# Performance work log

Hardware: AMD Instinct MI355X
Metric: run time of the kernel (lower is better)

Reference implementation:

```python
import jax, jax.numpy as jnp
import numpy as np

N_NODES = 100000
N_EDGES = 1600000
HID = 150
N_LAYERS = 5


def setup_inputs() -> dict:
    key = jax.random.key(0)
    ks = jax.random.split(key, 7)
    s = 1.0 / np.sqrt(HID)
    return {
        "x": jax.random.normal(ks[0], (N_NODES, HID), dtype=jnp.float32),
        "weight": jax.random.uniform(ks[1], (N_LAYERS, HID, HID), jnp.float32, -s, s),
        "w_ih": jax.random.uniform(ks[2], (3 * HID, HID), jnp.float32, -s, s),
        "w_hh": jax.random.uniform(ks[3], (3 * HID, HID), jnp.float32, -s, s),
        "b_ih": jax.random.uniform(ks[4], (3 * HID,), jnp.float32, -s, s),
        "b_hh": jax.random.uniform(ks[5], (3 * HID,), jnp.float32, -s, s),
        "edge_index": jax.random.randint(ks[6], (2, N_EDGES), 0, N_NODES, dtype=jnp.int32),
    }


def _gru_cell(inp, h, w_ih, w_hh, b_ih, b_hh):
    # torch.nn.GRUCell math
    gi = inp @ w_ih.T + b_ih            # [N, 3H]
    gh = h @ w_hh.T + b_hh              # [N, 3H]
    i_r, i_z, i_n = jnp.split(gi, 3, axis=-1)
    h_r, h_z, h_n = jnp.split(gh, 3, axis=-1)
    r = jax.nn.sigmoid(i_r + h_r)
    z = jax.nn.sigmoid(i_z + h_z)
    n = jnp.tanh(i_n + r * h_n)
    return (1.0 - z) * n + z * h


def reference(x, weight, w_ih, w_hh, b_ih, b_hh, edge_index):
    # GatedGraphConv: h'_i = GRU( sum_{j->i} (h_j @ W_l), h_i ), repeated num_layers times
    src, dst = edge_index[0], edge_index[1]
    n_nodes = x.shape[0]
    h = x
    for l in range(weight.shape[0]):
        m = h @ weight[l]                                        # [N, H] transform
        aggr = jax.ops.segment_sum(m[src], dst, num_segments=n_nodes)  # scatter-add over edges
        h = _gru_cell(aggr, h, w_ih, w_hh, b_ih, b_hh)
    return h
```

## Files before the change

kernel.cpp:

```cpp
#include <hip/hip_runtime.h>
#include <hip/hip_bf16.h>
#include <cmath>

#define HID 150
#define NN 100000
#define NE 1600000
#define NL 5
#define G3 (3*HID)
#define KP 320
#define NP 640
#define KS 10
#define BM 64
#define HSTEPS 20
#define HS_BF (20*64*8)

#define NPBSH 9
#define NBK 196
#define CAPL 64
#define CAPG 10240
#define CHUNK 4096
#define BPAD 16

typedef __hip_bfloat16 bf16;
using short8 = __attribute__((ext_vector_type(8))) short;
using f32x4  = __attribute__((ext_vector_type(4))) float;

static __device__ __forceinline__ unsigned short bf_bits(float v) {
    __hip_bfloat16 h = __float2bfloat16(v);
    return *reinterpret_cast<unsigned short*>(&h);
}

static __device__ __forceinline__ float blo(unsigned int p) {
    return __uint_as_float((p & 0xffffu) << 16);
}
static __device__ __forceinline__ float bhi(unsigned int p) {
    return __uint_as_float(p & 0xffff0000u);
}

static __device__ __forceinline__ void gld_lds16(const void* g, void* l) {
    __builtin_amdgcn_global_load_lds(
        (const __attribute__((address_space(1))) void*)g,
        (__attribute__((address_space(3))) void*)l, 16, 0, 0);
}

__global__ void build_wfrag(const float* __restrict__ W, const float* __restrict__ w_ih,
                            const float* __restrict__ w_hh, const float* __restrict__ b_ih,
                            const float* __restrict__ b_hh, bf16* __restrict__ wfrag) {
    int idx = blockIdx.x * 256 + threadIdx.x;
    if (idx >= NL * KP * NP) return;
    int j = idx % NP;
    int k = (idx / NP) % KP;
    int l = idx / (NP * KP);
    int sec = j / 160;
    int f = j - sec * 160;
    float v = 0.f;
    if (f < HID) {
        if (k < HID) {
            if (sec < 3) {
                const float* Wl = W + (size_t)l * HID * HID + (size_t)k * HID;
                const float* wr = w_ih + (size_t)(sec * HID + f) * HID;
                float acc = 0.f;
                for (int t = 0; t < HID; ++t) acc += Wl[t] * wr[t];
                v = acc;
            }
        } else if (k == HID) {
            v = (sec == 0) ? b_ih[f] + b_hh[f]
              : (sec == 1) ? b_ih[HID + f] + b_hh[HID + f]
              : (sec == 2) ? b_ih[2 * HID + f]
                           : b_hh[2 * HID + f];
        } else if (k >= 160 && k < 160 + HID) {
            int kk = k - 160;
            if (sec == 0)      v = w_hh[(size_t)f * HID + kk];
            else if (sec == 1) v = w_hh[(size_t)(HID + f) * HID + kk];
            else if (sec == 3) v = w_hh[(size_t)(2 * HID + f) * HID + kk];
        }
    }
    int kstep = k >> 5, kq = (k >> 3) & 3, ki = k & 7;
    int half = sec >> 1, s2 = sec & 1;
    int fgroup = f >> 4, nl = j & 15;
    int tl = s2 * 10 + fgroup;
    int lane = kq * 16 + nl;
    size_t addr = ((((size_t)(l * KS + kstep) * 2 + half) * 20 + tl) * 64 + lane) * 8 + ki;
    wfrag[addr] = __float2bfloat16(v);
}

__global__ __launch_bounds__(256)
void bin_edges(const int* __restrict__ ei, int* __restrict__ bcnt,
               unsigned int* __restrict__ bbuf) {
    __shared__ int lcnt[NBK];
    __shared__ unsigned int lstage[NBK * CAPL];
    int t = threadIdx.x;
    for (int i = t; i < NBK; i += 256) lcnt[i] = 0;
    __syncthreads();
    int e0 = blockIdx.x * CHUNK;
#pragma unroll
    for (int it = 0; it < CHUNK / 256; ++it) {
        int e = e0 + it * 256 + t;
        if (e < NE) {
            int src = ei[e], dst = ei[NE + e];
            int b = dst >> NPBSH;
            unsigned int v = (unsigned int)src | ((unsigned int)(dst & 511) << 17);
            int li = atomicAdd(&lcnt[b], 1);
            if (li < CAPL) {
                lstage[b * CAPL + li] = v;
            } else {
                int gp = atomicAdd(&bcnt[b * BPAD], 1);
                if (gp < CAPG) bbuf[(size_t)b * CAPG + gp] = v;
            }
        }
    }
    __syncthreads();
    int wave = t >> 6, lane = t & 63;
    for (int b = wave; b < NBK; b += 4) {
        int cnt = lcnt[b];
        if (cnt > CAPL) cnt = CAPL;
        if (cnt == 0) continue;
        int base = 0;
        if (lane == 0) base = atomicAdd(&bcnt[b * BPAD], cnt);
        base = __shfl(base, 0, 64);
        if (lane < cnt && base + lane < CAPG)
            bbuf[(size_t)b * CAPG + base + lane] = lstage[b * CAPL + lane];
    }
}

__global__ __launch_bounds__(256)
void csr_from_buckets(const int* __restrict__ bcnt, const unsigned int* __restrict__ bbuf,
                      int* __restrict__ off, int* __restrict__ csr) {
    __shared__ int hist[512];
    __shared__ int s[256];
    int b = blockIdx.x, t = threadIdx.x;
    hist[t] = 0;
    hist[256 + t] = 0;
    int base = 0;
    for (int i = 0; i < b; ++i) {
        int c = bcnt[i * BPAD];
        base += (c > CAPG) ? CAPG : c;
    }
    int cnt = bcnt[b * BPAD];
    if (cnt > CAPG) cnt = CAPG;
    __syncthreads();
    for (int i = t; i < cnt; i += 256) {
        unsigned int v = bbuf[(size_t)b * CAPG + i];
        atomicAdd(&hist[v >> 17], 1);
    }
    __syncthreads();
    int a0 = hist[2 * t], a1 = hist[2 * t + 1];
    int tsum = a0 + a1;
    s[t] = tsum;
    __syncthreads();
    for (int d = 1; d < 256; d <<= 1) {
        int u = (t >= d) ? s[t - d] : 0;
        __syncthreads();
        s[t] += u;
        __syncthreads();
    }
    int tb = base + s[t] - tsum;
    hist[2 * t] = tb;
    hist[2 * t + 1] = tb + a0;
    int node = (b << NPBSH) + 2 * t;
    if (node < NN) off[node] = tb;
    if (node + 1 < NN) off[node + 1] = tb + a0;
    if (b == NBK - 1 && t == 255) off[NN] = base + s[255];
    __syncthreads();
    for (int i = t; i < cnt; i += 256) {
        unsigned int v = bbuf[(size_t)b * CAPG + i];
        int p = atomicAdd(&hist[v >> 17], 1);
        csr[p] = (int)(v & 0x1FFFFu);
    }
}

__global__ void init_h(const float* __restrict__ x, bf16* __restrict__ Abuf) {
    size_t i = (size_t)blockIdx.x * 256 + threadIdx.x;
    if (i >= (size_t)NN * HID) return;
    int m = (int)(i / HID), f = (int)(i - (size_t)m * HID);
    Abuf[(size_t)m * KP + 160 + f] = __float2bfloat16(x[i]);
}

__global__ void aggregate(bf16* __restrict__ Abuf, const int* __restrict__ off,
                          const int* __restrict__ csr) {
    int node = (blockIdx.x * blockDim.x + threadIdx.x) >> 6;
    int lane = threadIdx.x & 63;
    if (node >= NN) return;
    int e0 = off[node], e1 = off[node + 1];
    float a0 = 0.f, a1 = 0.f, b0 = 0.f, b1 = 0.f;
    bool tail = lane < 11;
    int e = e0;
    for (; e + 4 <= e1; e += 4) {
        const unsigned int* r0 = (const unsigned int*)(Abuf + (size_t)csr[e]     * KP + 160);
        const unsigned int* r1 = (const unsigned int*)(Abuf + (size_t)csr[e + 1] * KP + 160);
        const unsigned int* r2 = (const unsigned int*)(Abuf + (size_t)csr[e + 2] * KP + 160);
        const unsigned int* r3 = (const unsigned int*)(Abuf + (size_t)csr[e + 3] * KP + 160);
        unsigned int p0 = r0[lane], p1 = r1[lane], p2 = r2[lane], p3 = r3[lane];
        unsigned int q0 = 0, q1 = 0, q2 = 0, q3 = 0;
        if (tail) { q0 = r0[64 + lane]; q1 = r1[64 + lane]; q2 = r2[64 + lane]; q3 = r3[64 + lane]; }
        a0 += blo(p0) + blo(p1) + blo(p2) + blo(p3);
        a1 += bhi(p0) + bhi(p1) + bhi(p2) + bhi(p3);
        b0 += blo(q0) + blo(q1) + blo(q2) + blo(q3);
        b1 += bhi(q0) + bhi(q1) + bhi(q2) + bhi(q3);
    }
    for (; e < e1; ++e) {
        const unsigned int* r = (const unsigned int*)(Abuf + (size_t)csr[e] * KP + 160);
        unsigned int p = r[lane];
        unsigned int q = tail ? r[64 + lane] : 0;
        a0 += blo(p); a1 += bhi(p);
        b0 += blo(q); b1 += bhi(q);
    }
    unsigned int* out = (unsigned int*)(Abuf + (size_t)node * KP);
    out[lane] = (unsigned int)bf_bits(a0) | ((unsigned int)bf_bits(a1) << 16);
    if (tail) out[64 + lane] = (unsigned int)bf_bits(b0) | ((unsigned int)bf_bits(b1) << 16);
    if (lane < 5) out[75 + lane] = (lane == 0) ? 0x00003F80u : 0u;
}

__global__ __launch_bounds__(256, 2)
void gemm_gru(const bf16* __restrict__ Abuf, const bf16* __restrict__ wfrag_l,
              float* __restrict__ h_out, bf16* __restrict__ Abuf_w, int last) {
    __shared__ __align__(16) bf16 Bs[3][HS_BF];
    __shared__ __align__(16) bf16 As3[3][BM * 32];
    int tid = threadIdx.x;
    int wave = tid >> 6, lane = tid & 63;
    int mh = wave >> 1, nh = wave & 1;
    int row0 = blockIdx.x * BM;

    const char* gbase = (const char*)(Abuf + (size_t)row0 * KP);
    int ar = tid >> 2, aq = tid & 3;

    auto stageB = [&](int hs) {
        const char* gb = (const char*)(wfrag_l + (size_t)hs * HS_BF);
        char* lb = (char*)Bs[hs % 3];
#pragma unroll
        for (int it = 0; it < 5; ++it) {
            int c = it * 256 + tid;
            gld_lds16(gb + (size_t)c * 16, lb + (size_t)c * 16);
        }
    };
    auto stageA = [&](int ks) {
        gld_lds16(gbase + (size_t)ar * (KP * 2) + ks * 64 + aq * 16,
                  (char*)As3[ks % 3] + (size_t)tid * 16);
    };

    stageB(0); stageA(0); stageB(1); stageA(1);

    f32x4 acc[2][20];
#pragma unroll
    for (int mt = 0; mt < 2; ++mt)
#pragma unroll
        for (int t = 0; t < 20; ++t) acc[mt][t] = (f32x4){0.f, 0.f, 0.f, 0.f};

    int col = lane & 15, q = lane >> 4;
    short8 a0, a1;
#pragma unroll
    for (int hs = 0; hs < HSTEPS; ++hs) {
        if (hs < 18)       asm volatile("s_waitcnt vmcnt(6)" ::: "memory");
        else if (hs == 18) asm volatile("s_waitcnt vmcnt(5)" ::: "memory");
        else               asm volatile("s_waitcnt vmcnt(0)" ::: "memory");
        __builtin_amdgcn_s_barrier();
        __builtin_amdgcn_sched_barrier(0);

        int ks = hs >> 1, half = hs & 1, cur = hs % 3;
        if (half == 0) {
            const bf16* Ak = As3[ks % 3];
            a0 = *(const short8*)(Ak + ((mh * 32 + col) * 32 + q * 8));
            a1 = *(const short8*)(Ak + ((mh * 32 + 16 + col) * 32 + q * 8));
        }
#pragma unroll
        for (int g = 0; g < 5; ++g) {
#pragma unroll
            for (int s2 = 0; s2 < 2; ++s2) {
                int tl = s2 * 10 + nh * 5 + g;
                short8 b = *(const short8*)(Bs[cur] + ((size_t)(tl * 64 + lane) * 8));
                int t = g * 4 + half * 2 + s2;
                acc[0][t] = __builtin_amdgcn_mfma_f32_16x16x32_bf16(a0, b, acc[0][t], 0, 0, 0);
                acc[1][t] = __builtin_amdgcn_mfma_f32_16x16x32_bf16(a1, b, acc[1][t], 0, 0, 0);
            }
        }
        if (hs + 2 < HSTEPS) stageB(hs + 2);
        if (half == 1 && ks + 2 < KS) stageA(ks + 2);
    }

    int qrow = q * 4;
    bf16* Cs = &Bs[0][0];
#pragma unroll
    for (int mt = 0; mt < 2; ++mt) {
#pragma unroll
        for (int g = 0; g < 5; ++g) {
            int f = (nh * 5 + g) * 16 + col;
            if (f < HID) {
                f32x4 ar4 = acc[mt][g * 4 + 0], az = acc[mt][g * 4 + 1];
                f32x4 an = acc[mt][g * 4 + 2], ah = acc[mt][g * 4 + 3];
#pragma unroll
                for (int v = 0; v < 4; ++v) {
                    int rl = mh * 32 + mt * 16 + qrow + v;
                    float hp = __bfloat162float(Abuf[(size_t)(row0 + rl) * KP + 160 + f]);
                    float r = 1.f / (1.f + __expf(-ar4[v]));
                    float z = 1.f / (1.f + __expf(-az[v]));
                    float n = tanhf(an[v] + r * ah[v]);
                    float ho = (1.f - z) * n + z * hp;
                    if (last) {
                        int m = row0 + rl;
                        if (m < NN) h_out[(size_t)m * HID + f] = ho;
                    } else {
                        Cs[rl * 160 + f] = __float2bfloat16(ho);
                    }
                }
            }
        }
    }
    if (!last) {
        __syncthreads();
        const unsigned int* src = (const unsigned int*)Cs;
        for (int i = tid; i < 64 * 75; i += 256) {
            int r = i / 75, dw = i - r * 75;
            ((unsigned int*)(Abuf_w + (size_t)(row0 + r) * KP + 160))[dw] =
                src[r * 80 + dw];
        }
    }
}

extern "C" void kernel_launch(void* const* d_in, const int* in_sizes, int n_in,
                              void* d_out, int out_size, void* d_ws, size_t ws_size,
                              hipStream_t stream) {
    const float* x      = (const float*)d_in[0];
    const float* weight = (const float*)d_in[1];
    const float* w_ih   = (const float*)d_in[2];
    const float* w_hh   = (const float*)d_in[3];
    const float* b_ih   = (const float*)d_in[4];
    const float* b_hh   = (const float*)d_in[5];
    const int*   ei     = (const int*)d_in[6];
    float* h = (float*)d_out;

    const int nblk = (NN + BM - 1) / BM;
    const size_t NNP = (size_t)nblk * BM;
    char* p = (char*)d_ws;
    auto alloc = [&](size_t bytes) { char* r = p; p += (bytes + 255) & ~255ull; return r; };
    int*  off   = (int*)alloc((size_t)(NN + 1) * 4);
    int*  csr   = (int*)alloc((size_t)NE * 4);
    int*  bcnt  = (int*)alloc((size_t)NBK * BPAD * 4);
    unsigned int* bbuf = (unsigned int*)alloc((size_t)NBK * CAPG * 4);
    bf16* wfrag = (bf16*)alloc((size_t)NL * KS * 2 * HS_BF * 2);
    bf16* Abuf  = (bf16*)alloc((NNP + BM) * (size_t)KP * 2);

    hipMemsetAsync(bcnt, 0, (size_t)NBK * BPAD * 4, stream);
    build_wfrag<<<(NL * KP * NP + 255) / 256, 256, 0, stream>>>(weight, w_ih, w_hh, b_ih, b_hh, wfrag);
    bin_edges<<<(NE + CHUNK - 1) / CHUNK, 256, 0, stream>>>(ei, bcnt, bbuf);
    csr_from_buckets<<<NBK, 256, 0, stream>>>(bcnt, bbuf, off, csr);
    init_h<<<(int)(((size_t)NN * HID + 255) / 256), 256, 0, stream>>>(x, Abuf);

    for (int l = 0; l < NL; ++l) {
        aggregate<<<(NN * 64 + 255) / 256, 256, 0, stream>>>(Abuf, off, csr);
        gemm_gru<<<nblk, 256, 0, stream>>>(Abuf, wfrag + (size_t)l * KS * 2 * HS_BF,
                                           h, Abuf, (l == NL - 1) ? 1 : 0);
    }
}
```

Baseline: 1.111 ms.

## Double GEMM-GRU tile to 128 rows with 512 threads and pairwise B staging

Raises the gemm_gru row tile from 64 to 128 and the block from 256 to 512 threads, so each staged weight slice feeds twice as many rows. Weight fragments are now staged two half-steps at a time, which halves the number of barriers and waitcnts in the main loop. tanhf is replaced by an exp-based formula. The larger LDS footprint and one block per CU reduce occupancy, and the wave-to-tile mapping (mh from wave>>1) must now cover 8 waves correctly.

```diff
diff --git a/kernel.cpp b/kernel.cpp
--- a/kernel.cpp
+++ b/kernel.cpp
@@ -10,7 +10,7 @@
 #define KP 320
 #define NP 640
 #define KS 10
-#define BM 64
+#define BM 128
 #define HSTEPS 20
 #define HS_BF (20*64*8)
 
@@ -211,10 +211,10 @@
     if (lane < 5) out[75 + lane] = (lane == 0) ? 0x00003F80u : 0u;
 }
 
-__global__ __launch_bounds__(256, 2)
+__global__ __launch_bounds__(512, 1)
 void gemm_gru(const bf16* __restrict__ Abuf, const bf16* __restrict__ wfrag_l,
               float* __restrict__ h_out, bf16* __restrict__ Abuf_w, int last) {
-    __shared__ __align__(16) bf16 Bs[3][HS_BF];
+    __shared__ __align__(16) bf16 Bs[6][HS_BF];
     __shared__ __align__(16) bf16 As3[3][BM * 32];
     int tid = threadIdx.x;
     int wave = tid >> 6, lane = tid & 63;
@@ -222,23 +222,22 @@
     int row0 = blockIdx.x * BM;
 
     const char* gbase = (const char*)(Abuf + (size_t)row0 * KP);
-    int ar = tid >> 2, aq = tid & 3;
-
-    auto stageB = [&](int hs) {
-        const char* gb = (const char*)(wfrag_l + (size_t)hs * HS_BF);
-        char* lb = (char*)Bs[hs % 3];
+
+    auto stagePair = [&](int pp) {
+        const char* gb = (const char*)(wfrag_l + (size_t)(pp * 2) * HS_BF);
+        char* lb = (char*)Bs[(pp % 3) * 2];
 #pragma unroll
         for (int it = 0; it < 5; ++it) {
-            int c = it * 256 + tid;
+            int c = it * 512 + tid;
             gld_lds16(gb + (size_t)c * 16, lb + (size_t)c * 16);
         }
     };
     auto stageA = [&](int ks) {
-        gld_lds16(gbase + (size_t)ar * (KP * 2) + ks * 64 + aq * 16,
+        gld_lds16(gbase + (size_t)(tid >> 2) * (KP * 2) + ks * 64 + (tid & 3) * 16,
                   (char*)As3[ks % 3] + (size_t)tid * 16);
     };
 
-    stageB(0); stageA(0); stageB(1); stageA(1);
+    stagePair(0); stageA(0); stagePair(1); stageA(1);
 
     f32x4 acc[2][20];
 #pragma unroll
@@ -250,32 +249,32 @@
     short8 a0, a1;
 #pragma unroll
     for (int hs = 0; hs < HSTEPS; ++hs) {
-        if (hs < 18)       asm volatile("s_waitcnt vmcnt(6)" ::: "memory");
-        else if (hs == 18) asm volatile("s_waitcnt vmcnt(5)" ::: "memory");
-        else               asm volatile("s_waitcnt vmcnt(0)" ::: "memory");
-        __builtin_amdgcn_s_barrier();
-        __builtin_amdgcn_sched_barrier(0);
-
-        int ks = hs >> 1, half = hs & 1, cur = hs % 3;
+        int p2 = hs >> 1, half = hs & 1;
         if (half == 0) {
-            const bf16* Ak = As3[ks % 3];
+            if (hs < 18) asm volatile("s_waitcnt vmcnt(6)" ::: "memory");
+            else         asm volatile("s_waitcnt vmcnt(0)" ::: "memory");
+            __builtin_amdgcn_s_barrier();
+            __builtin_amdgcn_sched_barrier(0);
+            if (p2 < 8) { stagePair(p2 + 2); stageA(p2 + 2); }
+            const bf16* Ak = As3[p2 % 3];
             a0 = *(const short8*)(Ak + ((mh * 32 + col) * 32 + q * 8));
             a1 = *(const short8*)(Ak + ((mh * 32 + 16 + col) * 32 + q * 8));
         }
+        const bf16* Bb = Bs[(p2 % 3) * 2 + half];
 #pragma unroll
         for (int g = 0; g < 5; ++g) {
 #pragma unroll
             for (int s2 = 0; s2 < 2; ++s2) {
                 int tl = s2 * 10 + nh * 5 + g;
-                short8 b = *(const short8*)(Bs[cur] + ((size_t)(tl * 64 + lane) * 8));
+                short8 b = *(const short8*)(Bb + ((size_t)(tl * 64 + lane) * 8));
                 int t = g * 4 + half * 2 + s2;
                 acc[0][t] = __builtin_amdgcn_mfma_f32_16x16x32_bf16(a0, b, acc[0][t], 0, 0, 0);
                 acc[1][t] = __builtin_amdgcn_mfma_f32_16x16x32_bf16(a1, b, acc[1][t], 0, 0, 0);
             }
         }
-        if (hs + 2 < HSTEPS) stageB(hs + 2);
-        if (half == 1 && ks + 2 < KS) stageA(ks + 2);
-    }
+    }
+
+    if (!last) __syncthreads();
 
     int qrow = q * 4;
     bf16* Cs = &Bs[0][0];
@@ -293,7 +292,8 @@
                     float hp = __bfloat162float(Abuf[(size_t)(row0 + rl) * KP + 160 + f]);
                     float r = 1.f / (1.f + __expf(-ar4[v]));
                     float z = 1.f / (1.f + __expf(-az[v]));
-                    float n = tanhf(an[v] + r * ah[v]);
+                    float e2 = __expf(2.f * (an[v] + r * ah[v]));
+                    float n = 1.f - 2.f / (e2 + 1.f);
                     float ho = (1.f - z) * n + z * hp;
                     if (last) {
                         int m = row0 + rl;
@@ -308,10 +308,10 @@
     if (!last) {
         __syncthreads();
         const unsigned int* src = (const unsigned int*)Cs;
-        for (int i = tid; i < 64 * 75; i += 256) {
-            int r = i / 75, dw = i - r * 75;
-            ((unsigned int*)(Abuf_w + (size_t)(row0 + r) * KP + 160))[dw] =
-                src[r * 80 + dw];
+        for (int i = tid; i < 128 * 75; i += 512) {
+            int r2 = i / 75, dw = i - r2 * 75;
+            ((unsigned int*)(Abuf_w + (size_t)(row0 + r2) * KP + 160))[dw] =
+                src[r2 * 80 + dw];
         }
     }
 }
@@ -347,7 +347,7 @@
 
     for (int l = 0; l < NL; ++l) {
         aggregate<<<(NN * 64 + 255) / 256, 256, 0, stream>>>(Abuf, off, csr);
-        gemm_gru<<<nblk, 256, 0, stream>>>(Abuf, wfrag + (size_t)l * KS * 2 * HS_BF,
+        gemm_gru<<<nblk, 512, 0, stream>>>(Abuf, wfrag + (size_t)l * KS * 2 * HS_BF,
                                            h, Abuf, (l == NL - 1) ? 1 : 0);
     }
 }
```

After: 1.157 ms. 4.1% more time.

## Fuse edge aggregation into GEMM+GRU kernel with ping-pong hidden buffers

Applied to the files above, without the earlier changes.

Merges the separate aggregate kernel into the GEMM/GRU kernel. Each block gathers and sums neighbor rows for its 64 nodes directly into LDS, then runs the MFMA GEMM with the aggregated half of A read from LDS and the hidden half held in registers. The hidden state moves to a compact 160-wide bf16 buffer, double-buffered across layers to avoid read/write races, and the gather loop is unrolled to 8 edges. This removes the global round trip of the aggregated matrix and one launch per layer. In exchange, the latency-bound gather now runs inside a high-register, LDS-heavy kernel, which may hurt occupancy and latency hiding, and the weight prefetch overlaps only the start of the gather.

```diff
diff --git a/kernel.cpp b/kernel.cpp
--- a/kernel.cpp
+++ b/kernel.cpp
@@ -6,13 +6,13 @@
 #define NN 100000
 #define NE 1600000
 #define NL 5
-#define G3 (3*HID)
+#define NP 640
 #define KP 320
-#define NP 640
 #define KS 10
 #define BM 64
 #define HSTEPS 20
 #define HS_BF (20*64*8)
+#define HROW 160
 
 #define NPBSH 9
 #define NBK 196
@@ -169,60 +169,34 @@
     }
 }
 
-__global__ void init_h(const float* __restrict__ x, bf16* __restrict__ Abuf) {
+__global__ void init_h(const float* __restrict__ x, bf16* __restrict__ hb0, int nrows) {
     size_t i = (size_t)blockIdx.x * 256 + threadIdx.x;
-    if (i >= (size_t)NN * HID) return;
-    int m = (int)(i / HID), f = (int)(i - (size_t)m * HID);
-    Abuf[(size_t)m * KP + 160 + f] = __float2bfloat16(x[i]);
-}
-
-__global__ void aggregate(bf16* __restrict__ Abuf, const int* __restrict__ off,
-                          const int* __restrict__ csr) {
-    int node = (blockIdx.x * blockDim.x + threadIdx.x) >> 6;
-    int lane = threadIdx.x & 63;
-    if (node >= NN) return;
-    int e0 = off[node], e1 = off[node + 1];
-    float a0 = 0.f, a1 = 0.f, b0 = 0.f, b1 = 0.f;
-    bool tail = lane < 11;
-    int e = e0;
-    for (; e + 4 <= e1; e += 4) {
-        const unsigned int* r0 = (const unsigned int*)(Abuf + (size_t)csr[e]     * KP + 160);
-        const unsigned int* r1 = (const unsigned int*)(Abuf + (size_t)csr[e + 1] * KP + 160);
-        const unsigned int* r2 = (const unsigned int*)(Abuf + (size_t)csr[e + 2] * KP + 160);
-        const unsigned int* r3 = (const unsigned int*)(Abuf + (size_t)csr[e + 3] * KP + 160);
-        unsigned int p0 = r0[lane], p1 = r1[lane], p2 = r2[lane], p3 = r3[lane];
-        unsigned int q0 = 0, q1 = 0, q2 = 0, q3 = 0;
-        if (tail) { q0 = r0[64 + lane]; q1 = r1[64 + lane]; q2 = r2[64 + lane]; q3 = r3[64 + lane]; }
-        a0 += blo(p0) + blo(p1) + blo(p2) + blo(p3);
-        a1 += bhi(p0) + bhi(p1) + bhi(p2) + bhi(p3);
-        b0 += blo(q0) + blo(q1) + blo(q2) + blo(q3);
-        b1 += bhi(q0) + bhi(q1) + bhi(q2) + bhi(q3);
-    }
-    for (; e < e1; ++e) {
-        const unsigned int* r = (const unsigned int*)(Abuf + (size_t)csr[e] * KP + 160);
-        unsigned int p = r[lane];
-        unsigned int q = tail ? r[64 + lane] : 0;
-        a0 += blo(p); a1 += bhi(p);
-        b0 += blo(q); b1 += bhi(q);
-    }
-    unsigned int* out = (unsigned int*)(Abuf + (size_t)node * KP);
-    out[lane] = (unsigned int)bf_bits(a0) | ((unsigned int)bf_bits(a1) << 16);
-    if (tail) out[64 + lane] = (unsigned int)bf_bits(b0) | ((unsigned int)bf_bits(b1) << 16);
-    if (lane < 5) out[75 + lane] = (lane == 0) ? 0x00003F80u : 0u;
+    if (i >= (size_t)nrows * HROW) return;
+    int m = (int)(i / HROW), f = (int)(i - (size_t)m * HROW);
+    float v = (m < NN && f < HID) ? x[(size_t)m * HID + f] : 0.f;
+    hb0[i] = __float2bfloat16(v);
 }
 
 __global__ __launch_bounds__(256, 2)
-void gemm_gru(const bf16* __restrict__ Abuf, const bf16* __restrict__ wfrag_l,
-              float* __restrict__ h_out, bf16* __restrict__ Abuf_w, int last) {
+void layer_fused(const bf16* __restrict__ hb_r, bf16* __restrict__ hb_w,
+                 const bf16* __restrict__ wfrag_l, const int* __restrict__ off,
+                 const int* __restrict__ csr, float* __restrict__ h_out, int last) {
+    __shared__ __align__(16) bf16 Ag[BM * HROW];
     __shared__ __align__(16) bf16 Bs[3][HS_BF];
-    __shared__ __align__(16) bf16 As3[3][BM * 32];
     int tid = threadIdx.x;
     int wave = tid >> 6, lane = tid & 63;
     int mh = wave >> 1, nh = wave & 1;
     int row0 = blockIdx.x * BM;
-
-    const char* gbase = (const char*)(Abuf + (size_t)row0 * KP);
-    int ar = tid >> 2, aq = tid & 3;
+    int col = lane & 15, q = lane >> 4;
+
+    const bf16* hrow0 = hb_r + (size_t)(row0 + mh * 32 + col) * HROW;
+    const bf16* hrow1 = hrow0 + (size_t)16 * HROW;
+    short8 aH0[5], aH1[5];
+#pragma unroll
+    for (int k5 = 0; k5 < 5; ++k5) {
+        aH0[k5] = *(const short8*)(hrow0 + k5 * 32 + q * 8);
+        aH1[k5] = *(const short8*)(hrow1 + k5 * 32 + q * 8);
+    }
 
     auto stageB = [&](int hs) {
         const char* gb = (const char*)(wfrag_l + (size_t)hs * HS_BF);
@@ -233,12 +207,63 @@
             gld_lds16(gb + (size_t)c * 16, lb + (size_t)c * 16);
         }
     };
-    auto stageA = [&](int ks) {
-        gld_lds16(gbase + (size_t)ar * (KP * 2) + ks * 64 + aq * 16,
-                  (char*)As3[ks % 3] + (size_t)tid * 16);
-    };
-
-    stageB(0); stageA(0); stageB(1); stageA(1);
+    stageB(0); stageB(1);
+
+    bool tailq = lane < 11;
+    for (int i = 0; i < 16; ++i) {
+        int rl = wave * 16 + i;
+        int node = row0 + rl;
+        int e0 = 0, e1 = 0;
+        if (node < NN) { e0 = off[node]; e1 = off[node + 1]; }
+        float s0 = 0.f, s1 = 0.f, t0 = 0.f, t1 = 0.f;
+        int e = e0;
+        for (; e + 8 <= e1; e += 8) {
+            const unsigned int* r0 = (const unsigned int*)(hb_r + (size_t)csr[e]     * HROW);
+            const unsigned int* r1 = (const unsigned int*)(hb_r + (size_t)csr[e + 1] * HROW);
+            const unsigned int* r2 = (const unsigned int*)(hb_r + (size_t)csr[e + 2] * HROW);
+            const unsigned int* r3 = (const unsigned int*)(hb_r + (size_t)csr[e + 3] * HROW);
+            const unsigned int* r4 = (const unsigned int*)(hb_r + (size_t)csr[e + 4] * HROW);
+            const unsigned int* r5 = (const unsigned int*)(hb_r + (size_t)csr[e + 5] * HROW);
+            const unsigned int* r6 = (const unsigned int*)(hb_r + (size_t)csr[e + 6] * HROW);
+            const unsigned int* r7 = (const unsigned int*)(hb_r + (size_t)csr[e + 7] * HROW);
+            unsigned int p0 = r0[lane], p1 = r1[lane], p2 = r2[lane], p3 = r3[lane];
+            unsigned int p4 = r4[lane], p5 = r5[lane], p6 = r6[lane], p7 = r7[lane];
+            unsigned int q0 = 0, q1 = 0, q2 = 0, q3 = 0, q4 = 0, q5 = 0, q6 = 0, q7 = 0;
+            if (tailq) {
+                q0 = r0[64 + lane]; q1 = r1[64 + lane]; q2 = r2[64 + lane]; q3 = r3[64 + lane];
+                q4 = r4[64 + lane]; q5 = r5[64 + lane]; q6 = r6[64 + lane]; q7 = r7[64 + lane];
+            }
+            s0 += blo(p0) + blo(p1) + blo(p2) + blo(p3) + blo(p4) + blo(p5) + blo(p6) + blo(p7);
+            s1 += bhi(p0) + bhi(p1) + bhi(p2) + bhi(p3) + bhi(p4) + bhi(p5) + bhi(p6) + bhi(p7);
+            t0 += blo(q0) + blo(q1) + blo(q2) + blo(q3) + blo(q4) + blo(q5) + blo(q6) + blo(q7);
+            t1 += bhi(q0) + bhi(q1) + bhi(q2) + bhi(q3) + bhi(q4) + bhi(q5) + bhi(q6) + bhi(q7);
+        }
+        for (; e + 4 <= e1; e += 4) {
+            const unsigned int* r0 = (const unsigned int*)(hb_r + (size_t)csr[e]     * HROW);
+            const unsigned int* r1 = (const unsigned int*)(hb_r + (size_t)csr[e + 1] * HROW);
+            const unsigned int* r2 = (const unsigned int*)(hb_r + (size_t)csr[e + 2] * HROW);
+            const unsigned int* r3 = (const unsigned int*)(hb_r + (size_t)csr[e + 3] * HROW);
+            unsigned int p0 = r0[lane], p1 = r1[lane], p2 = r2[lane], p3 = r3[lane];
+            unsigned int q0 = 0, q1 = 0, q2 = 0, q3 = 0;
+            if (tailq) { q0 = r0[64 + lane]; q1 = r1[64 + lane]; q2 = r2[64 + lane]; q3 = r3[64 + lane]; }
+            s0 += blo(p0) + blo(p1) + blo(p2) + blo(p3);
+            s1 += bhi(p0) + bhi(p1) + bhi(p2) + bhi(p3);
+            t0 += blo(q0) + blo(q1) + blo(q2) + blo(q3);
+            t1 += bhi(q0) + bhi(q1) + bhi(q2) + bhi(q3);
+        }
+        for (; e < e1; ++e) {
+            const unsigned int* r = (const unsigned int*)(hb_r + (size_t)csr[e] * HROW);
+            unsigned int p = r[lane];
+            unsigned int qv = tailq ? r[64 + lane] : 0;
+            s0 += blo(p); s1 += bhi(p);
+            t0 += blo(qv); t1 += bhi(qv);
+        }
+        unsigned int* outp = (unsigned int*)(Ag + (size_t)rl * HROW);
+        outp[lane] = (unsigned int)bf_bits(s0) | ((unsigned int)bf_bits(s1) << 16);
+        if (tailq) outp[64 + lane] = (unsigned int)bf_bits(t0) | ((unsigned int)bf_bits(t1) << 16);
+        if (lane < 5) outp[75 + lane] = (lane == 0) ? 0x00003F80u : 0u;
+    }
+    __syncthreads();
 
     f32x4 acc[2][20];
 #pragma unroll
@@ -246,39 +271,41 @@
 #pragma unroll
         for (int t = 0; t < 20; ++t) acc[mt][t] = (f32x4){0.f, 0.f, 0.f, 0.f};
 
-    int col = lane & 15, q = lane >> 4;
-    short8 a0, a1;
+    short8 a0v, a1v;
 #pragma unroll
     for (int hs = 0; hs < HSTEPS; ++hs) {
-        if (hs < 18)       asm volatile("s_waitcnt vmcnt(6)" ::: "memory");
-        else if (hs == 18) asm volatile("s_waitcnt vmcnt(5)" ::: "memory");
-        else               asm volatile("s_waitcnt vmcnt(0)" ::: "memory");
+        if (hs < 19) asm volatile("s_waitcnt vmcnt(5)" ::: "memory");
+        else         asm volatile("s_waitcnt vmcnt(0)" ::: "memory");
         __builtin_amdgcn_s_barrier();
         __builtin_amdgcn_sched_barrier(0);
 
-        int ks = hs >> 1, half = hs & 1, cur = hs % 3;
+        int ks = hs >> 1, half = hs & 1;
         if (half == 0) {
-            const bf16* Ak = As3[ks % 3];
-            a0 = *(const short8*)(Ak + ((mh * 32 + col) * 32 + q * 8));
-            a1 = *(const short8*)(Ak + ((mh * 32 + 16 + col) * 32 + q * 8));
-        }
+            if (ks < 5) {
+                a0v = *(const short8*)(Ag + (size_t)(mh * 32 + col) * HROW + ks * 32 + q * 8);
+                a1v = *(const short8*)(Ag + (size_t)(mh * 32 + 16 + col) * HROW + ks * 32 + q * 8);
+            } else {
+                a0v = aH0[ks - 5];
+                a1v = aH1[ks - 5];
+            }
+        }
+        const bf16* Bb = Bs[hs % 3];
 #pragma unroll
         for (int g = 0; g < 5; ++g) {
 #pragma unroll
             for (int s2 = 0; s2 < 2; ++s2) {
                 int tl = s2 * 10 + nh * 5 + g;
-                short8 b = *(const short8*)(Bs[cur] + ((size_t)(tl * 64 + lane) * 8));
+                short8 b = *(const short8*)(Bb + ((size_t)(tl * 64 + lane) * 8));
                 int t = g * 4 + half * 2 + s2;
-                acc[0][t] = __builtin_amdgcn_mfma_f32_16x16x32_bf16(a0, b, acc[0][t], 0, 0, 0);
-                acc[1][t] = __builtin_amdgcn_mfma_f32_16x16x32_bf16(a1, b, acc[1][t], 0, 0, 0);
+                acc[0][t] = __builtin_amdgcn_mfma_f32_16x16x32_bf16(a0v, b, acc[0][t], 0, 0, 0);
+                acc[1][t] = __builtin_amdgcn_mfma_f32_16x16x32_bf16(a1v, b, acc[1][t], 0, 0, 0);
             }
         }
         if (hs + 2 < HSTEPS) stageB(hs + 2);
-        if (half == 1 && ks + 2 < KS) stageA(ks + 2);
     }
 
     int qrow = q * 4;
-    bf16* Cs = &Bs[0][0];
+    bf16* Cs = Ag;
 #pragma unroll
     for (int mt = 0; mt < 2; ++mt) {
 #pragma unroll
@@ -290,7 +317,7 @@
 #pragma unroll
                 for (int v = 0; v < 4; ++v) {
                     int rl = mh * 32 + mt * 16 + qrow + v;
-                    float hp = __bfloat162float(Abuf[(size_t)(row0 + rl) * KP + 160 + f]);
+                    float hp = __bfloat162float(hb_r[(size_t)(row0 + rl) * HROW + f]);
                     float r = 1.f / (1.f + __expf(-ar4[v]));
                     float z = 1.f / (1.f + __expf(-az[v]));
                     float n = tanhf(an[v] + r * ah[v]);
@@ -299,7 +326,7 @@
                         int m = row0 + rl;
                         if (m < NN) h_out[(size_t)m * HID + f] = ho;
                     } else {
-                        Cs[rl * 160 + f] = __float2bfloat16(ho);
+                        Cs[(size_t)rl * HROW + f] = __float2bfloat16(ho);
                     }
                 }
             }
@@ -308,11 +335,8 @@
     if (!last) {
         __syncthreads();
         const unsigned int* src = (const unsigned int*)Cs;
-        for (int i = tid; i < 64 * 75; i += 256) {
-            int r = i / 75, dw = i - r * 75;
-            ((unsigned int*)(Abuf_w + (size_t)(row0 + r) * KP + 160))[dw] =
-                src[r * 80 + dw];
-        }
+        unsigned int* dst = (unsigned int*)hb_w + (size_t)row0 * 80;
+        for (int i = tid; i < BM * 80; i += 256) dst[i] = src[i];
     }
 }
 
@@ -329,7 +353,7 @@
     float* h = (float*)d_out;
 
     const int nblk = (NN + BM - 1) / BM;
-    const size_t NNP = (size_t)nblk * BM;
+    const int nrows = nblk * BM;
     char* p = (char*)d_ws;
     auto alloc = [&](size_t bytes) { char* r = p; p += (bytes + 255) & ~255ull; return r; };
     int*  off   = (int*)alloc((size_t)(NN + 1) * 4);
@@ -337,17 +361,20 @@
     int*  bcnt  = (int*)alloc((size_t)NBK * BPAD * 4);
     unsigned int* bbuf = (unsigned int*)alloc((size_t)NBK * CAPG * 4);
     bf16* wfrag = (bf16*)alloc((size_t)NL * KS * 2 * HS_BF * 2);
-    bf16* Abuf  = (bf16*)alloc((NNP + BM) * (size_t)KP * 2);
+    bf16* hb0   = (bf16*)alloc((size_t)nrows * HROW * 2);
+    bf16* hb1   = (bf16*)alloc((size_t)nrows * HROW * 2);
 
     hipMemsetAsync(bcnt, 0, (size_t)NBK * BPAD * 4, stream);
     build_wfrag<<<(NL * KP * NP + 255) / 256, 256, 0, stream>>>(weight, w_ih, w_hh, b_ih, b_hh, wfrag);
     bin_edges<<<(NE + CHUNK - 1) / CHUNK, 256, 0, stream>>>(ei, bcnt, bbuf);
     csr_from_buckets<<<NBK, 256, 0, stream>>>(bcnt, bbuf, off, csr);
-    init_h<<<(int)(((size_t)NN * HID + 255) / 256), 256, 0, stream>>>(x, Abuf);
-
+    init_h<<<(int)(((size_t)nrows * HROW + 255) / 256), 256, 0, stream>>>(x, hb0, nrows);
+
+    bf16* hr = hb0;
+    bf16* hw = hb1;
     for (int l = 0; l < NL; ++l) {
-        aggregate<<<(NN * 64 + 255) / 256, 256, 0, stream>>>(Abuf, off, csr);
-        gemm_gru<<<nblk, 256, 0, stream>>>(Abuf, wfrag + (size_t)l * KS * 2 * HS_BF,
-                                           h, Abuf, (l == NL - 1) ? 1 : 0);
-    }
-}
+        layer_fused<<<nblk, 256, 0, stream>>>(hr, hw, wfrag + (size_t)l * KS * 2 * HS_BF,
+                                              off, csr, h, (l == NL - 1) ? 1 : 0);
+        bf16* tmp = hr; hr = hw; hw = tmp;
+    }
+}
```

After: 1.609 ms. 44.8% more time.
